# Optimization experiments

Hardware: AMD Instinct MI355X
Metric: run time of the kernel (lower is better)

Reference implementation:

```python
import jax, jax.numpy as jnp
import numpy as np

H = 8          # attention heads
EPS = 1e-5     # LayerNorm eps (torch default)
B, T, E = 8, 1024, 128
D, DI, N, DC, R = 512, 1024, 16, 4, 32   # d_model, d_inner, d_state, d_conv, dt_rank
NT, NM = 6, 8                            # transformer layers, mamba layers
FF = 2048                                # transformer dim_feedforward (torch default)


def setup_inputs():
    key = jax.random.key(0)
    ks = iter(jax.random.split(key, 48))
    def rn(shape, scale=0.05):
        return jax.random.normal(next(ks), shape, jnp.float32) * scale
    return {
        "emb":      jax.random.normal(next(ks), (B, T, E), jnp.float32),
        # TransformerEncoder (6 post-norm layers), params stacked on leading layer dim
        "t_wqkv":   rn((NT, 3 * E, E)), "t_bqkv": jnp.zeros((NT, 3 * E), jnp.float32),
        "t_wo":     rn((NT, E, E)),     "t_bo":   jnp.zeros((NT, E), jnp.float32),
        "t_ln1w":   jnp.ones((NT, E), jnp.float32),  "t_ln1b": jnp.zeros((NT, E), jnp.float32),
        "t_w1":     rn((NT, FF, E)),    "t_b1":   jnp.zeros((NT, FF), jnp.float32),
        "t_w2":     rn((NT, E, FF)),    "t_b2":   jnp.zeros((NT, E), jnp.float32),
        "t_ln2w":   jnp.ones((NT, E), jnp.float32),  "t_ln2b": jnp.zeros((NT, E), jnp.float32),
        # Linear(emb_dim -> d_model)
        "w_in":     rn((D, E)), "b_in": jnp.zeros((D,), jnp.float32),
        # MambaBlocks (8 raw Mamba layers, no residual/norm), stacked
        "m_inproj": rn((NM, 2 * DI, D)),
        "m_convw":  rn((NM, DI, DC), 0.2), "m_convb": jnp.zeros((NM, DI), jnp.float32),
        "m_xproj":  rn((NM, R + 2 * N, DI)),
        "m_dtw":    rn((NM, DI, R), 0.1),
        "m_dtb":    jax.random.uniform(next(ks), (NM, DI), jnp.float32, -6.0, -3.0),
        "m_Alog":   jnp.log(jnp.tile(jnp.arange(1, N + 1, dtype=jnp.float32), (NM, DI, 1))),
        "m_D":      jnp.ones((NM, DI), jnp.float32),
        "m_outproj": rn((NM, D, DI)),
        # Linear(d_model -> emb_dim)
        "w_out":    rn((E, D)), "b_out": jnp.zeros((E,), jnp.float32),
    }


def _ln(x, w, b):
    mu = jnp.mean(x, -1, keepdims=True)
    var = jnp.var(x, -1, keepdims=True)
    return (x - mu) * jax.lax.rsqrt(var + EPS) * w + b


def _tlayer(x, p):
    wqkv, bqkv, wo, bo, ln1w, ln1b, w1, b1, w2, b2, ln2w, ln2b = p
    qkv = x @ wqkv.T + bqkv                        # (B,T,3E)
    q, k, v = jnp.split(qkv, 3, axis=-1)
    def heads(t):                                  # (B,T,E) -> (B,H,T,E//H)
        return t.reshape(B, T, H, E // H).transpose(0, 2, 1, 3)
    q, k, v = heads(q), heads(k), heads(v)
    scores = jnp.einsum("bhqd,bhkd->bhqk", q, k) / jnp.sqrt(jnp.float32(E // H))
    attn = jax.nn.softmax(scores, axis=-1)
    o = jnp.einsum("bhqk,bhkd->bhqd", attn, v).transpose(0, 2, 1, 3).reshape(B, T, E)
    x = _ln(x + o @ wo.T + bo, ln1w, ln1b)         # post-norm (torch default)
    ff = jax.nn.relu(x @ w1.T + b1) @ w2.T + b2
    return _ln(x + ff, ln2w, ln2b)


def _mamba_layer(x, p):
    inproj, convw, convb, xproj, dtw, dtb, Alog, Dp, outproj = p
    xz = x @ inproj.T                              # (B,T,2*DI)
    xi, z = jnp.split(xz, 2, axis=-1)
    # causal depthwise conv1d, kernel DC, left-padded
    xp = jnp.pad(xi, ((0, 0), (DC - 1, 0), (0, 0)))
    conv = sum(xp[:, k:k + T, :] * convw[:, k] for k in range(DC)) + convb
    xi = jax.nn.silu(conv)
    dbc = xi @ xproj.T                             # (B,T,R+2N)
    dt_r, Bt, Ct = dbc[..., :R], dbc[..., R:R + N], dbc[..., R + N:]
    dt = jax.nn.softplus(dt_r @ dtw.T + dtb)       # (B,T,DI)
    A = -jnp.exp(Alog)                             # (DI,N)
    def step(h, inputs):
        dt_t, B_t, C_t, x_t = inputs               # (B,DI),(B,N),(B,N),(B,DI)
        dA = jnp.exp(dt_t[:, :, None] * A)         # (B,DI,N)
        h = h * dA + (dt_t * x_t)[:, :, None] * B_t[:, None, :]
        y = jnp.einsum("bdn,bn->bd", h, C_t)
        return h, y
    h0 = jnp.zeros((B, DI, N), x.dtype)
    seq = (dt.transpose(1, 0, 2), Bt.transpose(1, 0, 2),
           Ct.transpose(1, 0, 2), xi.transpose(1, 0, 2))
    _, ys = jax.lax.scan(step, h0, seq)            # ys: (T,B,DI)
    y = ys.transpose(1, 0, 2) + Dp * xi
    y = y * jax.nn.silu(z)
    return y @ outproj.T                           # (B,T,D)


def reference(emb, t_wqkv, t_bqkv, t_wo, t_bo, t_ln1w, t_ln1b, t_w1, t_b1, t_w2, t_b2,
              t_ln2w, t_ln2b, w_in, b_in, m_inproj, m_convw, m_convb, m_xproj, m_dtw,
              m_dtb, m_Alog, m_D, m_outproj, w_out, b_out):
    x = emb
    tparams = (t_wqkv, t_bqkv, t_wo, t_bo, t_ln1w, t_ln1b, t_w1, t_b1, t_w2, t_b2, t_ln2w, t_ln2b)
    for i in range(NT):
        x = _tlayer(x, tuple(p[i] for p in tparams))
    x = x @ w_in.T + b_in                          # (B,T,D)
    mparams = (m_inproj, m_convw, m_convb, m_xproj, m_dtw, m_dtb, m_Alog, m_D, m_outproj)
    for i in range(NM):
        x = _mamba_layer(x, tuple(p[i] for p in mparams))
    return x @ w_out.T + b_out                     # (B,T,E)
```

## Files before the change

### kernel.cpp

```cpp
#include <hip/hip_runtime.h>
#include <math.h>

#define HB 8
#define TT 1024
#define NSTATE 16
#define NTT 6
#define NMM 8
#define MM (HB*TT)
#define EPSV 1e-5f
#define CHUNK 64
#define NCH (TT/CHUNK)
#define LSTR 72
#define AKS 128
#define VSTR 132

typedef _Float16 f16x8 __attribute__((ext_vector_type(8)));
typedef _Float16 f16x4 __attribute__((ext_vector_type(4)));
typedef float f32x4_t __attribute__((ext_vector_type(4)));

static __device__ inline void split8(const float4 a, const float4 b,
                                     f16x8& h, f16x8& l)
{
  float x[8] = {a.x, a.y, a.z, a.w, b.x, b.y, b.z, b.w};
#pragma unroll
  for (int i = 0; i < 8; i++) {
    _Float16 hi = (_Float16)x[i];
    h[i] = hi;
    l[i] = (_Float16)(x[i] - (float)hi);
  }
}

template<int TN>
__global__ __launch_bounds__(256) void gemm_mfma_t(
    const float* __restrict__ A, int lda,
    const float* __restrict__ W,
    const float* __restrict__ bias,
    float* __restrict__ C,
    float* __restrict__ P,
    int N, int K, int S, int act)
{
  __shared__ _Float16 As[128 * LSTR];
  __shared__ _Float16 Bs[TN * LSTR];
  const int tid = threadIdx.x;
  const int m0 = blockIdx.y * 128;
  const int n0 = blockIdx.x * TN;
  const int z = blockIdx.z;
  const int kchunk = K / S;
  const int kb = z * kchunk;
  const int ke = kb + kchunk;

  const int lr = tid >> 1;
  const int lh = tid & 1;
  const int lane = tid & 63;
  const int w = tid >> 6;
  const int quad = lane >> 4;
  const int l16 = lane & 15;

  const float* Arow = A + (size_t)(m0 + lr) * lda + lh * 16;
  _Float16* Adst = &As[lr * LSTR + lh * 16];

  constexpr int MI = (TN == 128) ? 4 : 2;
  const int w0 = (TN == 128) ? (w & 1) : w;
  const int w1 = (TN == 128) ? (w >> 1) : 0;
  const int rowbase = (TN == 128) ? w0 * 64 : w0 * 32;

  f32x4_t acc[MI][4];
#pragma unroll
  for (int i = 0; i < MI; i++)
#pragma unroll
    for (int j = 0; j < 4; j++)
#pragma unroll
      for (int r = 0; r < 4; r++) acc[i][j][r] = 0.f;

  const _Float16* ab = &As[(rowbase + l16) * LSTR + quad * 8];
  const _Float16* bb = &Bs[(w1 * 64 + l16) * LSTR + quad * 8];

  const float* Wrow;
  _Float16* Bdst;
  if (TN == 128) {
    Wrow = W + (size_t)(n0 + lr) * K + lh * 16;
    Bdst = &Bs[lr * LSTR + lh * 16];
  } else {
    const int br = tid >> 2;
    const int bo = (tid & 3) * 8;
    Wrow = W + (size_t)(n0 + br) * K + bo;
    Bdst = &Bs[br * LSTR + bo];
  }

  for (int k0 = kb; k0 < ke; k0 += 32) {
    float4 a0 = *(const float4*)&Arow[k0];
    float4 a1 = *(const float4*)&Arow[k0 + 4];
    float4 a2 = *(const float4*)&Arow[k0 + 8];
    float4 a3 = *(const float4*)&Arow[k0 + 12];
    float4 b0 = *(const float4*)&Wrow[k0];
    float4 b1 = *(const float4*)&Wrow[k0 + 4];
    float4 b2, b3;
    if (TN == 128) {
      b2 = *(const float4*)&Wrow[k0 + 8];
      b3 = *(const float4*)&Wrow[k0 + 12];
    }
    __syncthreads();
    {
      f16x8 h, l;
      split8(a0, a1, h, l);
      *(f16x8*)&Adst[0] = h; *(f16x8*)&Adst[32] = l;
      split8(a2, a3, h, l);
      *(f16x8*)&Adst[8] = h; *(f16x8*)&Adst[40] = l;
      split8(b0, b1, h, l);
      *(f16x8*)&Bdst[0] = h; *(f16x8*)&Bdst[32] = l;
      if (TN == 128) {
        split8(b2, b3, h, l);
        *(f16x8*)&Bdst[8] = h; *(f16x8*)&Bdst[40] = l;
      }
    }
    __syncthreads();

    f16x8 bh[4], bl[4];
#pragma unroll
    for (int ni = 0; ni < 4; ni++) {
      bh[ni] = *(const f16x8*)&bb[ni * 16 * LSTR];
      bl[ni] = *(const f16x8*)&bb[ni * 16 * LSTR + 32];
    }
#pragma unroll
    for (int mi = 0; mi < MI; mi++) {
      f16x8 ah = *(const f16x8*)&ab[mi * 16 * LSTR];
      f16x8 al = *(const f16x8*)&ab[mi * 16 * LSTR + 32];
#pragma unroll
      for (int ni = 0; ni < 4; ni++) {
        acc[mi][ni] = __builtin_amdgcn_mfma_f32_16x16x32_f16(ah, bh[ni], acc[mi][ni], 0, 0, 0);
        acc[mi][ni] = __builtin_amdgcn_mfma_f32_16x16x32_f16(ah, bl[ni], acc[mi][ni], 0, 0, 0);
        acc[mi][ni] = __builtin_amdgcn_mfma_f32_16x16x32_f16(al, bh[ni], acc[mi][ni], 0, 0, 0);
      }
    }
  }

  float* dst = (S == 1) ? C : (P + (size_t)z * MM * N);
#pragma unroll
  for (int ni = 0; ni < 4; ni++) {
    const int n = n0 + w1 * 64 + ni * 16 + l16;
    const float bv = (S == 1 && bias) ? bias[n] : 0.f;
#pragma unroll
    for (int mi = 0; mi < MI; mi++) {
      const int mbase = m0 + rowbase + mi * 16 + quad * 4;
#pragma unroll
      for (int r = 0; r < 4; r++) {
        float v = acc[mi][ni][r] + bv;
        if (S == 1) {
          if (act == 1) v = fmaxf(v, 0.f);
          else if (act == 2) v = fmaxf(v, 0.f) + log1pf(__expf(-fabsf(v)));
        }
        dst[(size_t)(mbase + r) * N + n] = v;
      }
    }
  }
}

__global__ __launch_bounds__(256) void reduce_k(
    const float* __restrict__ P, const float* __restrict__ bias,
    float* __restrict__ C, int nmask, int S, int act, int stride4)
{
  const int idx = blockIdx.x * 256 + threadIdx.x;
  float4 a = *(const float4*)&P[(size_t)idx * 4];
  for (int z = 1; z < S; z++) {
    float4 p = *(const float4*)&P[(size_t)(idx + z * (size_t)stride4) * 4];
    a.x += p.x; a.y += p.y; a.z += p.z; a.w += p.w;
  }
  if (bias) {
    float4 bv = *(const float4*)&bias[(idx * 4) & nmask];
    a.x += bv.x; a.y += bv.y; a.z += bv.z; a.w += bv.w;
  }
  if (act == 1) {
    a.x = fmaxf(a.x, 0.f); a.y = fmaxf(a.y, 0.f);
    a.z = fmaxf(a.z, 0.f); a.w = fmaxf(a.w, 0.f);
  } else if (act == 2) {
    a.x = fmaxf(a.x, 0.f) + log1pf(__expf(-fabsf(a.x)));
    a.y = fmaxf(a.y, 0.f) + log1pf(__expf(-fabsf(a.y)));
    a.z = fmaxf(a.z, 0.f) + log1pf(__expf(-fabsf(a.z)));
    a.w = fmaxf(a.w, 0.f) + log1pf(__expf(-fabsf(a.w)));
  }
  *(float4*)&C[(size_t)idx * 4] = a;
}

__global__ __launch_bounds__(256) void attn_mfma_k(
    const float* __restrict__ qkv, float* __restrict__ o)
{
  __shared__ _Float16 Khi[AKS * 16], Klo[AKS * 16];
  __shared__ _Float16 Vthi[16 * VSTR], Vtlo[16 * VSTR];
  __shared__ float Pscr[4][16 * 18];

  const int tid = threadIdx.x;
  const int lane = tid & 63;
  const int wv = tid >> 6;
  const int quad = lane >> 4;
  const int l16 = lane & 15;
  const int qh = quad & 1;
  const int bh = blockIdx.y;
  const int b = bh >> 3;
  const int h = bh & 7;
  const int qb0 = blockIdx.x * 128;

  f16x8 qa[2];
#pragma unroll
  for (int u = 0; u < 2; u++) {
    const int qrow = qb0 + wv * 32 + u * 16 + l16;
    const float* qp = qkv + (size_t)(b * TT + qrow) * 384 + h * 16 + qh * 8;
    float4 x0 = *(const float4*)&qp[0];
    float4 x1 = *(const float4*)&qp[4];
    float xv[8] = {x0.x, x0.y, x0.z, x0.w, x1.x, x1.y, x1.z, x1.w};
#pragma unroll
    for (int j = 0; j < 8; j++) {
      float q = xv[j] * 0.25f;
      _Float16 hi = (_Float16)q;
      _Float16 lo = (_Float16)(q - (float)hi);
      qa[u][j] = (quad < 2) ? hi : lo;
    }
  }

  f32x4_t oacc[2];
  float lacc[2][4];
#pragma unroll
  for (int u = 0; u < 2; u++)
#pragma unroll
    for (int r = 0; r < 4; r++) { oacc[u][r] = 0.f; lacc[u][r] = 0.f; }

  float* Pw = &Pscr[wv][0];

  for (int ks = 0; ks < TT; ks += AKS) {
    __syncthreads();
    {
      const int key = tid >> 1, hf = tid & 1;
      const float* kp = qkv + (size_t)(b * TT + ks + key) * 384 + 128 + h * 16 + hf * 8;
      float4 k0 = *(const float4*)&kp[0];
      float4 k1 = *(const float4*)&kp[4];
      f16x8 vh, vl;
      split8(k0, k1, vh, vl);
      *(f16x8*)&Khi[key * 16 + hf * 8] = vh;
      *(f16x8*)&Klo[key * 16 + hf * 8] = vl;
      const float* vp = kp + 128;
      float4 v0 = *(const float4*)&vp[0];
      float4 v1 = *(const float4*)&vp[4];
      float vvv[8] = {v0.x, v0.y, v0.z, v0.w, v1.x, v1.y, v1.z, v1.w};
#pragma unroll
      for (int j = 0; j < 8; j++) {
        const int d = hf * 8 + j;
        _Float16 hi = (_Float16)vvv[j];
        Vthi[d * VSTR + key] = hi;
        Vtlo[d * VSTR + key] = (_Float16)(vvv[j] - (float)hi);
      }
    }
    __syncthreads();

    for (int kt = 0; kt < AKS; kt += 16) {
      f16x8 kfh = *(const f16x8*)&Khi[(kt + l16) * 16 + qh * 8];
      f16x8 kfl = *(const f16x8*)&Klo[(kt + l16) * 16 + qh * 8];
      const int vo = l16 * VSTR + kt + qh * 8;
      f16x4 va0 = *(const f16x4*)&Vthi[vo];
      f16x4 va1 = *(const f16x4*)&Vthi[vo + 4];
      f16x4 vb0 = *(const f16x4*)&Vtlo[vo];
      f16x4 vb1 = *(const f16x4*)&Vtlo[vo + 4];
      f16x8 vfh, vfl;
#pragma unroll
      for (int i = 0; i < 4; i++) {
        vfh[i] = va0[i]; vfh[4 + i] = va1[i];
        vfl[i] = vb0[i]; vfl[4 + i] = vb1[i];
      }

#pragma unroll
      for (int u = 0; u < 2; u++) {
        f32x4_t s;
#pragma unroll
        for (int r = 0; r < 4; r++) s[r] = 0.f;
        s = __builtin_amdgcn_mfma_f32_16x16x32_f16(qa[u], kfh, s, 0, 0, 0);
        s = __builtin_amdgcn_mfma_f32_16x16x32_f16(qa[u], kfl, s, 0, 0, 0);
        float p[4];
#pragma unroll
        for (int r = 0; r < 4; r++) {
          p[r] = __expf(s[r]);
          lacc[u][r] += p[r];
        }
        float* ps = Pw + (quad * 4) * 18 + l16;
        ps[0] = p[0]; ps[18] = p[1]; ps[36] = p[2]; ps[54] = p[3];
        __asm__ volatile("s_waitcnt lgkmcnt(0)" ::: "memory");
        const float* pr = Pw + l16 * 18 + qh * 8;
        f16x8 pa;
#pragma unroll
        for (int j = 0; j < 8; j++) {
          float pv = pr[j];
          _Float16 hi = (_Float16)pv;
          _Float16 lo = (_Float16)(pv - (float)hi);
          pa[j] = (quad < 2) ? hi : lo;
        }
        oacc[u] = __builtin_amdgcn_mfma_f32_16x16x32_f16(pa, vfh, oacc[u], 0, 0, 0);
        oacc[u] = __builtin_amdgcn_mfma_f32_16x16x32_f16(pa, vfl, oacc[u], 0, 0, 0);
        __asm__ volatile("s_waitcnt lgkmcnt(0)" ::: "memory");
      }
    }
  }

#pragma unroll
  for (int u = 0; u < 2; u++) {
#pragma unroll
    for (int r = 0; r < 4; r++) {
      float lv = lacc[u][r];
      lv += __shfl_xor(lv, 1);
      lv += __shfl_xor(lv, 2);
      lv += __shfl_xor(lv, 4);
      lv += __shfl_xor(lv, 8);
      const float inv = 1.f / lv;
      const int qrow = qb0 + wv * 32 + u * 16 + quad * 4 + r;
      o[(size_t)(b * TT + qrow) * 128 + h * 16 + l16] = oacc[u][r] * inv;
    }
  }
}

__global__ __launch_bounds__(256) void add_ln_k(
    const float* __restrict__ a, const float* __restrict__ bvec,
    const float* __restrict__ w, const float* __restrict__ bb,
    float* __restrict__ out)
{
  const int tid = threadIdx.x;
  const int wave = tid >> 6, lane = tid & 63;
  const size_t row = (size_t)blockIdx.x * 4 + wave;
  const float* pa = a + row * 128;
  const float* pb = bvec + row * 128;
  float v0 = pa[lane] + pb[lane];
  float v1 = pa[lane + 64] + pb[lane + 64];
  float s1 = v0 + v1, s2 = v0 * v0 + v1 * v1;
#pragma unroll
  for (int off = 32; off; off >>= 1) {
    s1 += __shfl_down(s1, off);
    s2 += __shfl_down(s2, off);
  }
  s1 = __shfl(s1, 0); s2 = __shfl(s2, 0);
  const float mean = s1 * (1.f / 128.f);
  const float var = s2 * (1.f / 128.f) - mean * mean;
  const float rs = rsqrtf(var + EPSV);
  out[row * 128 + lane]      = (v0 - mean) * rs * w[lane] + bb[lane];
  out[row * 128 + lane + 64] = (v1 - mean) * rs * w[lane + 64] + bb[lane + 64];
}

__global__ __launch_bounds__(256) void conv_silu_k(
    const float* __restrict__ xz, const float* __restrict__ cw,
    const float* __restrict__ cb, float* __restrict__ out)
{
  const int idx = blockIdx.x * 256 + threadIdx.x;
  const int di = idx & 1023;
  const int m = idx >> 10;
  const int t = m & (TT - 1);
  float acc = cb[di];
#pragma unroll
  for (int k = 0; k < 4; k++) {
    int tt = t + k - 3;
    if (tt >= 0) acc += xz[(size_t)(m + k - 3) * 2048 + di] * cw[di * 4 + k];
  }
  out[(size_t)m * 1024 + di] = acc / (1.f + __expf(-acc));
}

__global__ __launch_bounds__(64) void scan_partial_k(
    const float* __restrict__ dt,
    const float* __restrict__ dbc,
    const float* __restrict__ xi,
    const float* __restrict__ Alog,
    float* __restrict__ Pb, float* __restrict__ Sb)
{
  const int slice = blockIdx.x & 15;
  const int c = blockIdx.x >> 4;
  const int b = blockIdx.y;
  const int di = slice * 64 + threadIdx.x;

  float A[NSTATE];
#pragma unroll
  for (int n = 0; n < NSTATE; n++) A[n] = -__expf(Alog[di * NSTATE + n]);
  float h[NSTATE], P[NSTATE];
#pragma unroll
  for (int n = 0; n < NSTATE; n++) { h[n] = 0.f; P[n] = 1.f; }

  const size_t m0 = (size_t)b * TT + (size_t)c * CHUNK;
  for (int t = 0; t < CHUNK; t++) {
    const size_t m = m0 + t;
    const float dtv = dt[m * 1024 + di];
    const float xv  = xi[m * 1024 + di];
    const float dtx = dtv * xv;
#pragma unroll
    for (int n = 0; n < NSTATE; n++) {
      const float Bv = dbc[m * 64 + 32 + n];
      const float dA = __expf(dtv * A[n]);
      h[n] = h[n] * dA + dtx * Bv;
      P[n] *= dA;
    }
  }
  const size_t base = (((size_t)b * NCH + c) * NSTATE) * 1024 + di;
#pragma unroll
  for (int n = 0; n < NSTATE; n++) {
    Pb[base + (size_t)n * 1024] = P[n];
    Sb[base + (size_t)n * 1024] = h[n];
  }
}

__global__ __launch_bounds__(256) void scan_fix_k(
    float* __restrict__ Pb, const float* __restrict__ Sb)
{
  const int idx = blockIdx.x * 256 + threadIdx.x;
  const int b = idx >> 10;
  const int di = idx & 1023;
  float h[NSTATE];
#pragma unroll
  for (int n = 0; n < NSTATE; n++) h[n] = 0.f;
  for (int c = 0; c < NCH; c++) {
    const size_t base = (((size_t)b * NCH + c) * NSTATE) * 1024 + di;
    float P[NSTATE], S[NSTATE];
#pragma unroll
    for (int n = 0; n < NSTATE; n++) {
      P[n] = Pb[base + (size_t)n * 1024];
      S[n] = Sb[base + (size_t)n * 1024];
    }
#pragma unroll
    for (int n = 0; n < NSTATE; n++) {
      Pb[base + (size_t)n * 1024] = h[n];
      h[n] = P[n] * h[n] + S[n];
    }
  }
}

__global__ __launch_bounds__(64) void scan_final_k(
    const float* __restrict__ dt,
    const float* __restrict__ dbc,
    const float* __restrict__ xi,
    const float* __restrict__ xz,
    const float* __restrict__ Alog,
    const float* __restrict__ Dp,
    const float* __restrict__ Hin,
    float* __restrict__ Y)
{
  const int slice = blockIdx.x & 15;
  const int c = blockIdx.x >> 4;
  const int b = blockIdx.y;
  const int di = slice * 64 + threadIdx.x;

  float A[NSTATE];
#pragma unroll
  for (int n = 0; n < NSTATE; n++) A[n] = -__expf(Alog[di * NSTATE + n]);
  const float Dv = Dp[di];
  float h[NSTATE];
  const size_t hbase = (((size_t)b * NCH + c) * NSTATE) * 1024 + di;
#pragma unroll
  for (int n = 0; n < NSTATE; n++) h[n] = Hin[hbase + (size_t)n * 1024];

  const size_t m0 = (size_t)b * TT + (size_t)c * CHUNK;
  for (int t = 0; t < CHUNK; t++) {
    const size_t m = m0 + t;
    const float dtv = dt[m * 1024 + di];
    const float xv  = xi[m * 1024 + di];
    const float zv  = xz[m * 2048 + 1024 + di];
    const float dtx = dtv * xv;
    float y = 0.f;
#pragma unroll
    for (int n = 0; n < NSTATE; n++) {
      const float Bv = dbc[m * 64 + 32 + n];
      const float Cv = dbc[m * 64 + 48 + n];
      const float dA = __expf(dtv * A[n]);
      h[n] = h[n] * dA + dtx * Bv;
      y += h[n] * Cv;
    }
    y += Dv * xv;
    y *= zv / (1.f + __expf(-zv));
    Y[m * 1024 + di] = y;
  }
}

extern "C" void kernel_launch(void* const* d_in, const int* in_sizes, int n_in,
                              void* d_out, int out_size, void* d_ws, size_t ws_size,
                              hipStream_t stream)
{
  const float* emb      = (const float*)d_in[0];
  const float* t_wqkv   = (const float*)d_in[1];
  const float* t_bqkv   = (const float*)d_in[2];
  const float* t_wo     = (const float*)d_in[3];
  const float* t_bo     = (const float*)d_in[4];
  const float* t_ln1w   = (const float*)d_in[5];
  const float* t_ln1b   = (const float*)d_in[6];
  const float* t_w1     = (const float*)d_in[7];
  const float* t_b1     = (const float*)d_in[8];
  const float* t_w2     = (const float*)d_in[9];
  const float* t_b2     = (const float*)d_in[10];
  const float* t_ln2w   = (const float*)d_in[11];
  const float* t_ln2b   = (const float*)d_in[12];
  const float* w_in     = (const float*)d_in[13];
  const float* b_in     = (const float*)d_in[14];
  const float* m_inproj = (const float*)d_in[15];
  const float* m_convw  = (const float*)d_in[16];
  const float* m_convb  = (const float*)d_in[17];
  const float* m_xproj  = (const float*)d_in[18];
  const float* m_dtw    = (const float*)d_in[19];
  const float* m_dtb    = (const float*)d_in[20];
  const float* m_Alog   = (const float*)d_in[21];
  const float* m_D      = (const float*)d_in[22];
  const float* m_outproj= (const float*)d_in[23];
  const float* w_out    = (const float*)d_in[24];
  const float* b_out    = (const float*)d_in[25];

  float* ws = (float*)d_ws;
  float* X0   = ws;
  float* X1   = X0 + (size_t)MM * 512;
  float* Abuf = X1 + (size_t)MM * 512;
  float* Bf   = Abuf + (size_t)MM * 2048;
  float* Cf   = Bf + (size_t)MM * 1024;
  float* Yb   = Cf + (size_t)MM * 1024;
  float* Db   = Yb + (size_t)MM * 1024;

  dim3 blk(256);
  auto gemm = [&](const float* A, int lda, const float* W, const float* bias,
                  float* C, int N, int K, int act, int S, float* P, bool tn64) {
    dim3 g(N / (tn64 ? 64 : 128), MM / 128, S);
    if (tn64)
      hipLaunchKernelGGL(gemm_mfma_t<64>, g, blk, 0, stream,
                         A, lda, W, S == 1 ? bias : nullptr, C, P, N, K, S, act);
    else
      hipLaunchKernelGGL(gemm_mfma_t<128>, g, blk, 0, stream,
                         A, lda, W, S == 1 ? bias : nullptr, C, P, N, K, S, act);
    if (S > 1) {
      int stride4 = (MM * N) / 4;
      hipLaunchKernelGGL(reduce_k, dim3(stride4 / 256), blk, 0, stream,
                         P, bias, C, N - 1, S, act, stride4);
    }
  };

  const float* x = emb;
  for (int l = 0; l < NTT; l++) {
    gemm(x, 128, t_wqkv + (size_t)l * 384 * 128, t_bqkv + l * 384,
         Abuf, 384, 128, 0, 1, nullptr, false);
    hipLaunchKernelGGL(attn_mfma_k, dim3(TT / 128, HB * 8), blk, 0, stream,
                       Abuf, Yb);
    gemm(Yb, 128, t_wo + (size_t)l * 128 * 128, t_bo + l * 128,
         Cf, 128, 128, 0, 2, X1, true);
    hipLaunchKernelGGL(add_ln_k, dim3(MM / 4), blk, 0, stream,
                       x, Cf, t_ln1w + l * 128, t_ln1b + l * 128, X0);
    gemm(X0, 128, t_w1 + (size_t)l * 2048 * 128, t_b1 + l * 2048,
         Abuf, 2048, 128, 1, 1, nullptr, false);
    gemm(Abuf, 2048, t_w2 + (size_t)l * 128 * 2048, t_b2 + l * 128,
         Cf, 128, 2048, 0, 8, Yb, false);
    hipLaunchKernelGGL(add_ln_k, dim3(MM / 4), blk, 0, stream,
                       X0, Cf, t_ln2w + l * 128, t_ln2b + l * 128, X0);
    x = X0;
  }

  gemm(X0, 128, w_in, b_in, X1, 512, 128, 0, 1, nullptr, false);

  float* xc = X1;
  float* xo = X0;
  for (int l = 0; l < NMM; l++) {
    gemm(xc, 512, m_inproj + (size_t)l * 2048 * 512, nullptr,
         Abuf, 2048, 512, 0, 1, nullptr, false);
    hipLaunchKernelGGL(conv_silu_k, dim3(MM * 1024 / 256), blk, 0, stream,
                       Abuf, m_convw + (size_t)l * 1024 * 4, m_convb + l * 1024, Bf);
    gemm(Bf, 1024, m_xproj + (size_t)l * 64 * 1024, nullptr,
         Db, 64, 1024, 0, 4, xo, true);
    gemm(Db, 64, m_dtw + (size_t)l * 1024 * 32, m_dtb + l * 1024,
         Cf, 1024, 32, 2, 1, nullptr, false);

    float* Pb = xo;
    float* Sb = xo + (size_t)HB * NCH * NSTATE * 1024;
    hipLaunchKernelGGL(scan_partial_k, dim3(16 * NCH, HB), dim3(64), 0, stream,
                       Cf, Db, Bf, m_Alog + (size_t)l * 1024 * 16, Pb, Sb);
    hipLaunchKernelGGL(scan_fix_k, dim3(MM / 1024 * 4), blk, 0, stream, Pb, Sb);
    hipLaunchKernelGGL(scan_final_k, dim3(16 * NCH, HB), dim3(64), 0, stream,
                       Cf, Db, Bf, Abuf,
                       m_Alog + (size_t)l * 1024 * 16, m_D + l * 1024, Pb, Yb);

    gemm(Yb, 1024, m_outproj + (size_t)l * 512 * 1024, nullptr,
         xo, 512, 1024, 0, 2, Abuf, false);
    float* tmp = xc; xc = xo; xo = tmp;
  }

  gemm(xc, 512, w_out, b_out, (float*)d_out, 128, 512, 0, 4, Yb, false);
}
```

Baseline: 3.623 ms.

## Pre-split GEMM operands into swizzled fp16 hi/lo tiles loaded via global_load_lds

Instead of each GEMM converting fp32 A and W tiles into fp16 hi/lo pairs inside the main loop, producers (attention, layernorm, conv, scan, reduce, GEMM epilogue) now write their outputs directly in a pre-split, XOR-swizzled fp16 tile layout, and weights are split by separate split kernels. The GEMM then streams tiles straight into LDS with global_load_lds and does no conversion in its inner loop. The workspace is reorganized into aliased regions. This removes per-tile conversion ALU work and register staging, at the cost of extra split-kernel launches, double-written outputs, and delicate buffer aliasing.

```diff
diff --git a/kernel.cpp b/kernel.cpp
--- a/kernel.cpp
+++ b/kernel.cpp
@@ -10,7 +10,6 @@
 #define EPSV 1e-5f
 #define CHUNK 64
 #define NCH (TT/CHUNK)
-#define LSTR 72
 #define AKS 128
 #define VSTR 132
 
@@ -18,8 +17,8 @@
 typedef _Float16 f16x4 __attribute__((ext_vector_type(4)));
 typedef float f32x4_t __attribute__((ext_vector_type(4)));
 
-static __device__ inline void split8(const float4 a, const float4 b,
-                                     f16x8& h, f16x8& l)
+static __device__ __forceinline__ void split8(const float4 a, const float4 b,
+                                              f16x8& h, f16x8& l)
 {
   float x[8] = {a.x, a.y, a.z, a.w, b.x, b.y, b.z, b.w};
 #pragma unroll
@@ -30,34 +29,90 @@
   }
 }
 
+static __device__ __forceinline__ void gload16(const _Float16* g, _Float16* l)
+{
+  __builtin_amdgcn_global_load_lds(
+      (const __attribute__((address_space(1))) unsigned int*)g,
+      (__attribute__((address_space(3))) unsigned int*)l, 16, 0, 0);
+}
+
+static __device__ __forceinline__ void store_split(_Float16* __restrict__ dst,
+                                                   size_t row, int col, float v)
+{
+  const int cc = col & 31;
+  const size_t o = ((size_t)(col >> 5) * MM + row) * 64
+                 + (size_t)(((((cc >> 3) ^ ((int)row & 7)) * 8)) + (cc & 7));
+  _Float16 hi = (_Float16)v;
+  dst[o] = hi;
+  dst[o ^ (size_t)32] = (_Float16)(v - (float)hi);
+}
+
+static __device__ __forceinline__ void split_item(
+    const float* __restrict__ src, int lda, int rows,
+    _Float16* __restrict__ dst, int item)
+{
+  const int m = item % rows;
+  const int seg = item / rows;
+  const float* s = src + (size_t)m * lda + seg * 32;
+  _Float16* d = dst + (size_t)item * 64;
+  const int swz = m & 7;
+#pragma unroll
+  for (int g = 0; g < 4; g++) {
+    float4 x0 = *(const float4*)&s[g * 8];
+    float4 x1 = *(const float4*)&s[g * 8 + 4];
+    f16x8 h, l;
+    split8(x0, x1, h, l);
+    const int u = (g ^ swz) * 8;
+    *(f16x8*)&d[u] = h;
+    *(f16x8*)&d[u ^ 32] = l;
+  }
+}
+
+__global__ __launch_bounds__(256) void split_k(
+    const float* __restrict__ src, int lda, int rows,
+    _Float16* __restrict__ dst)
+{
+  split_item(src, lda, rows, dst, blockIdx.x * 256 + threadIdx.x);
+}
+
+__global__ __launch_bounds__(256) void split3_k(
+    const float* __restrict__ s0, int lda0, int rows0, _Float16* __restrict__ d0, int nb0,
+    const float* __restrict__ s1, int lda1, int rows1, _Float16* __restrict__ d1, int nb1,
+    const float* __restrict__ s2, int lda2, int rows2, _Float16* __restrict__ d2)
+{
+  const int bid = blockIdx.x;
+  if (bid < nb0) {
+    split_item(s0, lda0, rows0, d0, bid * 256 + threadIdx.x);
+  } else if (bid < nb0 + nb1) {
+    split_item(s1, lda1, rows1, d1, (bid - nb0) * 256 + threadIdx.x);
+  } else {
+    split_item(s2, lda2, rows2, d2, (bid - nb0 - nb1) * 256 + threadIdx.x);
+  }
+}
+
 template<int TN>
-__global__ __launch_bounds__(256) void gemm_mfma_t(
-    const float* __restrict__ A, int lda,
-    const float* __restrict__ W,
+__global__ __launch_bounds__(256, 4) void gemm_ps_t(
+    const _Float16* __restrict__ Ap, int astr,
+    const _Float16* __restrict__ Wp, int wstr,
     const float* __restrict__ bias,
     float* __restrict__ C,
     float* __restrict__ P,
+    _Float16* __restrict__ Cs,
     int N, int K, int S, int act)
 {
-  __shared__ _Float16 As[128 * LSTR];
-  __shared__ _Float16 Bs[TN * LSTR];
+  __shared__ __align__(16) _Float16 As[128 * 64];
+  __shared__ __align__(16) _Float16 Bs[TN * 64];
   const int tid = threadIdx.x;
-  const int m0 = blockIdx.y * 128;
-  const int n0 = blockIdx.x * TN;
-  const int z = blockIdx.z;
-  const int kchunk = K / S;
-  const int kb = z * kchunk;
-  const int ke = kb + kchunk;
-
-  const int lr = tid >> 1;
-  const int lh = tid & 1;
   const int lane = tid & 63;
   const int w = tid >> 6;
   const int quad = lane >> 4;
   const int l16 = lane & 15;
-
-  const float* Arow = A + (size_t)(m0 + lr) * lda + lh * 16;
-  _Float16* Adst = &As[lr * LSTR + lh * 16];
+  const int m0 = blockIdx.y * 128;
+  const int n0 = blockIdx.x * TN;
+  const int z = blockIdx.z;
+  const int nseg = K / 32;
+  const int segb = z * (nseg / S);
+  const int sege = segb + nseg / S;
 
   constexpr int MI = (TN == 128) ? 4 : 2;
   const int w0 = (TN == 128) ? (w & 1) : w;
@@ -72,59 +127,33 @@
 #pragma unroll
       for (int r = 0; r < 4; r++) acc[i][j][r] = 0.f;
 
-  const _Float16* ab = &As[(rowbase + l16) * LSTR + quad * 8];
-  const _Float16* bb = &Bs[(w1 * 64 + l16) * LSTR + quad * 8];
-
-  const float* Wrow;
-  _Float16* Bdst;
-  if (TN == 128) {
-    Wrow = W + (size_t)(n0 + lr) * K + lh * 16;
-    Bdst = &Bs[lr * LSTR + lh * 16];
-  } else {
-    const int br = tid >> 2;
-    const int bo = (tid & 3) * 8;
-    Wrow = W + (size_t)(n0 + br) * K + bo;
-    Bdst = &Bs[br * LSTR + bo];
-  }
-
-  for (int k0 = kb; k0 < ke; k0 += 32) {
-    float4 a0 = *(const float4*)&Arow[k0];
-    float4 a1 = *(const float4*)&Arow[k0 + 4];
-    float4 a2 = *(const float4*)&Arow[k0 + 8];
-    float4 a3 = *(const float4*)&Arow[k0 + 12];
-    float4 b0 = *(const float4*)&Wrow[k0];
-    float4 b1 = *(const float4*)&Wrow[k0 + 4];
-    float4 b2, b3;
-    if (TN == 128) {
-      b2 = *(const float4*)&Wrow[k0 + 8];
-      b3 = *(const float4*)&Wrow[k0 + 12];
-    }
+  const int sw8 = (quad ^ (l16 & 7)) * 8;
+  const int abase = (rowbase + l16) * 64 + sw8;
+  const int bbase = (w1 * 64 + l16) * 64 + sw8;
+  const int wave64 = tid & 192;
+
+  for (int seg = segb; seg < sege; seg++) {
+    const _Float16* At = Ap + ((size_t)seg * astr + m0) * 64;
+    const _Float16* Bt = Wp + ((size_t)seg * wstr + n0) * 64;
     __syncthreads();
-    {
-      f16x8 h, l;
-      split8(a0, a1, h, l);
-      *(f16x8*)&Adst[0] = h; *(f16x8*)&Adst[32] = l;
-      split8(a2, a3, h, l);
-      *(f16x8*)&Adst[8] = h; *(f16x8*)&Adst[40] = l;
-      split8(b0, b1, h, l);
-      *(f16x8*)&Bdst[0] = h; *(f16x8*)&Bdst[32] = l;
-      if (TN == 128) {
-        split8(b2, b3, h, l);
-        *(f16x8*)&Bdst[8] = h; *(f16x8*)&Bdst[40] = l;
-      }
-    }
+#pragma unroll
+    for (int j = 0; j < 4; j++)
+      gload16(At + (size_t)(j * 256 + tid) * 8, &As[(j * 256 + wave64) * 8]);
+#pragma unroll
+    for (int j = 0; j < TN / 32; j++)
+      gload16(Bt + (size_t)(j * 256 + tid) * 8, &Bs[(j * 256 + wave64) * 8]);
     __syncthreads();
 
     f16x8 bh[4], bl[4];
 #pragma unroll
     for (int ni = 0; ni < 4; ni++) {
-      bh[ni] = *(const f16x8*)&bb[ni * 16 * LSTR];
-      bl[ni] = *(const f16x8*)&bb[ni * 16 * LSTR + 32];
+      bh[ni] = *(const f16x8*)&Bs[bbase + ni * 1024];
+      bl[ni] = *(const f16x8*)&Bs[(bbase ^ 32) + ni * 1024];
     }
 #pragma unroll
     for (int mi = 0; mi < MI; mi++) {
-      f16x8 ah = *(const f16x8*)&ab[mi * 16 * LSTR];
-      f16x8 al = *(const f16x8*)&ab[mi * 16 * LSTR + 32];
+      f16x8 ah = *(const f16x8*)&As[abase + mi * 1024];
+      f16x8 al = *(const f16x8*)&As[(abase ^ 32) + mi * 1024];
 #pragma unroll
       for (int ni = 0; ni < 4; ni++) {
         acc[mi][ni] = __builtin_amdgcn_mfma_f32_16x16x32_f16(ah, bh[ni], acc[mi][ni], 0, 0, 0);
@@ -149,7 +178,12 @@
           if (act == 1) v = fmaxf(v, 0.f);
           else if (act == 2) v = fmaxf(v, 0.f) + log1pf(__expf(-fabsf(v)));
         }
-        dst[(size_t)(mbase + r) * N + n] = v;
+        const int row = mbase + r;
+        if (S == 1 && Cs) {
+          store_split(Cs, (size_t)row, n, v);
+        } else {
+          dst[(size_t)row * N + n] = v;
+        }
       }
     }
   }
@@ -157,12 +191,14 @@
 
 __global__ __launch_bounds__(256) void reduce_k(
     const float* __restrict__ P, const float* __restrict__ bias,
-    float* __restrict__ C, int nmask, int S, int act, int stride4)
+    float* __restrict__ C, _Float16* __restrict__ Cs,
+    _Float16* __restrict__ dta,
+    int nmask, int nshift, int S, int act, int stride4)
 {
   const int idx = blockIdx.x * 256 + threadIdx.x;
   float4 a = *(const float4*)&P[(size_t)idx * 4];
   for (int z = 1; z < S; z++) {
-    float4 p = *(const float4*)&P[(size_t)(idx + z * (size_t)stride4) * 4];
+    float4 p = *(const float4*)&P[(size_t)(idx + (size_t)z * stride4) * 4];
     a.x += p.x; a.y += p.y; a.z += p.z; a.w += p.w;
   }
   if (bias) {
@@ -178,11 +214,26 @@
     a.z = fmaxf(a.z, 0.f) + log1pf(__expf(-fabsf(a.z)));
     a.w = fmaxf(a.w, 0.f) + log1pf(__expf(-fabsf(a.w)));
   }
-  *(float4*)&C[(size_t)idx * 4] = a;
+  const int c0 = (idx * 4) & nmask;
+  const size_t row = (size_t)(idx * 4) >> nshift;
+  if (Cs) {
+    store_split(Cs, row, c0,     a.x);
+    store_split(Cs, row, c0 + 1, a.y);
+    store_split(Cs, row, c0 + 2, a.z);
+    store_split(Cs, row, c0 + 3, a.w);
+  } else {
+    *(float4*)&C[(size_t)idx * 4] = a;
+  }
+  if (dta && c0 < 32) {
+    store_split(dta, row, c0,     a.x);
+    store_split(dta, row, c0 + 1, a.y);
+    store_split(dta, row, c0 + 2, a.z);
+    store_split(dta, row, c0 + 3, a.w);
+  }
 }
 
 __global__ __launch_bounds__(256) void attn_mfma_k(
-    const float* __restrict__ qkv, float* __restrict__ o)
+    const float* __restrict__ qkv, _Float16* __restrict__ os)
 {
   __shared__ _Float16 Khi[AKS * 16], Klo[AKS * 16];
   __shared__ _Float16 Vthi[16 * VSTR], Vtlo[16 * VSTR];
@@ -308,7 +359,8 @@
       lv += __shfl_xor(lv, 8);
       const float inv = 1.f / lv;
       const int qrow = qb0 + wv * 32 + u * 16 + quad * 4 + r;
-      o[(size_t)(b * TT + qrow) * 128 + h * 16 + l16] = oacc[u][r] * inv;
+      const size_t m = (size_t)(b * TT + qrow);
+      store_split(os, m, h * 16 + l16, oacc[u][r] * inv);
     }
   }
 }
@@ -316,7 +368,7 @@
 __global__ __launch_bounds__(256) void add_ln_k(
     const float* __restrict__ a, const float* __restrict__ bvec,
     const float* __restrict__ w, const float* __restrict__ bb,
-    float* __restrict__ out)
+    float* __restrict__ out, _Float16* __restrict__ outs)
 {
   const int tid = threadIdx.x;
   const int wave = tid >> 6, lane = tid & 63;
@@ -335,13 +387,18 @@
   const float mean = s1 * (1.f / 128.f);
   const float var = s2 * (1.f / 128.f) - mean * mean;
   const float rs = rsqrtf(var + EPSV);
-  out[row * 128 + lane]      = (v0 - mean) * rs * w[lane] + bb[lane];
-  out[row * 128 + lane + 64] = (v1 - mean) * rs * w[lane + 64] + bb[lane + 64];
+  const float o0 = (v0 - mean) * rs * w[lane] + bb[lane];
+  const float o1 = (v1 - mean) * rs * w[lane + 64] + bb[lane + 64];
+  out[row * 128 + lane] = o0;
+  out[row * 128 + lane + 64] = o1;
+  store_split(outs, row, lane, o0);
+  store_split(outs, row, lane + 64, o1);
 }
 
 __global__ __launch_bounds__(256) void conv_silu_k(
     const float* __restrict__ xz, const float* __restrict__ cw,
-    const float* __restrict__ cb, float* __restrict__ out)
+    const float* __restrict__ cb, float* __restrict__ out,
+    _Float16* __restrict__ outs)
 {
   const int idx = blockIdx.x * 256 + threadIdx.x;
   const int di = idx & 1023;
@@ -353,7 +410,9 @@
     int tt = t + k - 3;
     if (tt >= 0) acc += xz[(size_t)(m + k - 3) * 2048 + di] * cw[di * 4 + k];
   }
-  out[(size_t)m * 1024 + di] = acc / (1.f + __expf(-acc));
+  const float y = acc / (1.f + __expf(-acc));
+  out[(size_t)m * 1024 + di] = y;
+  store_split(outs, (size_t)m, di, y);
 }
 
 __global__ __launch_bounds__(64) void scan_partial_k(
@@ -430,7 +489,7 @@
     const float* __restrict__ Alog,
     const float* __restrict__ Dp,
     const float* __restrict__ Hin,
-    float* __restrict__ Y)
+    _Float16* __restrict__ Y)
 {
   const int slice = blockIdx.x & 15;
   const int c = blockIdx.x >> 4;
@@ -464,7 +523,7 @@
     }
     y += Dv * xv;
     y *= zv / (1.f + __expf(-zv));
-    Y[m * 1024 + di] = y;
+    store_split(Y, m, di, y);
   }
 }
 
@@ -472,6 +531,7 @@
                               void* d_out, int out_size, void* d_ws, size_t ws_size,
                               hipStream_t stream)
 {
+  (void)in_sizes; (void)n_in; (void)out_size; (void)ws_size;
   const float* emb      = (const float*)d_in[0];
   const float* t_wqkv   = (const float*)d_in[1];
   const float* t_bqkv   = (const float*)d_in[2];
@@ -500,77 +560,116 @@
   const float* b_out    = (const float*)d_in[25];
 
   float* ws = (float*)d_ws;
-  float* X0   = ws;
-  float* X1   = X0 + (size_t)MM * 512;
-  float* Abuf = X1 + (size_t)MM * 512;
-  float* Bf   = Abuf + (size_t)MM * 2048;
-  float* Cf   = Bf + (size_t)MM * 1024;
-  float* Yb   = Cf + (size_t)MM * 1024;
-  float* Db   = Yb + (size_t)MM * 1024;
+  float* R1 = ws;
+  float* R2 = ws + (size_t)MM * 512;
+  float* R3 = ws + (size_t)MM * 1024;
+  float* R4 = ws + (size_t)MM * 3072;
+  float* R5 = ws + (size_t)MM * 4096;
+  float* R6 = ws + (size_t)MM * 5120;
+  float* R7 = ws + (size_t)MM * 6144;
+
+  _Float16* TWQKV = (_Float16*)R4;
+  _Float16* TWO   = TWQKV + (size_t)294912 * 2;
+  _Float16* TW1   = TWO   + (size_t)98304 * 2;
+  _Float16* TW2   = TW1   + (size_t)1572864 * 2;
+  _Float16* TWIN  = TW2   + (size_t)1572864 * 2;
+
+  _Float16* ASP1 = (_Float16*)R6;
+  _Float16* XIS  = (_Float16*)R6;
+  _Float16* DTA  = (_Float16*)R6;
+  _Float16* YSP  = (_Float16*)R6;
 
   dim3 blk(256);
-  auto gemm = [&](const float* A, int lda, const float* W, const float* bias,
-                  float* C, int N, int K, int act, int S, float* P, bool tn64) {
+  auto split = [&](const float* src, int lda, int rows, int K, _Float16* dst) {
+    hipLaunchKernelGGL(split_k, dim3(rows * (K / 32) / 256), blk, 0, stream,
+                       src, lda, rows, dst);
+  };
+  auto gemm = [&](const _Float16* Ap, const _Float16* Wp, int wstr,
+                  const float* bias, float* C, int N, int K, int act,
+                  int S, float* P, _Float16* Cs, _Float16* dta, bool tn64) {
     dim3 g(N / (tn64 ? 64 : 128), MM / 128, S);
     if (tn64)
-      hipLaunchKernelGGL(gemm_mfma_t<64>, g, blk, 0, stream,
-                         A, lda, W, S == 1 ? bias : nullptr, C, P, N, K, S, act);
+      hipLaunchKernelGGL(gemm_ps_t<64>, g, blk, 0, stream,
+                         Ap, MM, Wp, wstr, bias, C, P, Cs, N, K, S, act);
     else
-      hipLaunchKernelGGL(gemm_mfma_t<128>, g, blk, 0, stream,
-                         A, lda, W, S == 1 ? bias : nullptr, C, P, N, K, S, act);
+      hipLaunchKernelGGL(gemm_ps_t<128>, g, blk, 0, stream,
+                         Ap, MM, Wp, wstr, bias, C, P, Cs, N, K, S, act);
     if (S > 1) {
-      int stride4 = (MM * N) / 4;
+      int stride4 = (int)((size_t)MM * N / 4);
       hipLaunchKernelGGL(reduce_k, dim3(stride4 / 256), blk, 0, stream,
-                         P, bias, C, N - 1, S, act, stride4);
+                         P, bias, C, Cs, dta, N - 1, __builtin_ctz(N), S, act,
+                         stride4);
     }
   };
+
+  split(t_wqkv, 128,  2304,  128, TWQKV);
+  split(t_wo,   128,   768,  128, TWO);
+  split(t_w1,   128, 12288,  128, TW1);
+  split(t_w2,  2048,   768, 2048, TW2);
+  split(w_in,   128,   512,  128, TWIN);
+  split(emb,    128,    MM,  128, ASP1);
 
   const float* x = emb;
   for (int l = 0; l < NTT; l++) {
-    gemm(x, 128, t_wqkv + (size_t)l * 384 * 128, t_bqkv + l * 384,
-         Abuf, 384, 128, 0, 1, nullptr, false);
+    gemm(ASP1, TWQKV + (size_t)l * 384 * 64, 2304, t_bqkv + l * 384,
+         R3, 384, 128, 0, 1, nullptr, nullptr, nullptr, false);
     hipLaunchKernelGGL(attn_mfma_k, dim3(TT / 128, HB * 8), blk, 0, stream,
-                       Abuf, Yb);
-    gemm(Yb, 128, t_wo + (size_t)l * 128 * 128, t_bo + l * 128,
-         Cf, 128, 128, 0, 2, X1, true);
+                       R3, ASP1);
+    gemm(ASP1, TWO + (size_t)l * 128 * 64, 768, t_bo + l * 128,
+         R5, 128, 128, 0, 2, R2, nullptr, nullptr, true);
     hipLaunchKernelGGL(add_ln_k, dim3(MM / 4), blk, 0, stream,
-                       x, Cf, t_ln1w + l * 128, t_ln1b + l * 128, X0);
-    gemm(X0, 128, t_w1 + (size_t)l * 2048 * 128, t_b1 + l * 2048,
-         Abuf, 2048, 128, 1, 1, nullptr, false);
-    gemm(Abuf, 2048, t_w2 + (size_t)l * 128 * 2048, t_b2 + l * 128,
-         Cf, 128, 2048, 0, 8, Yb, false);
+                       x, R5, t_ln1w + l * 128, t_ln1b + l * 128, R1, ASP1);
+    gemm(ASP1, TW1 + (size_t)l * 2048 * 64, 12288, t_b1 + l * 2048,
+         R3, 2048, 128, 1, 1, nullptr, (_Float16*)R3, nullptr, false);
+    gemm((_Float16*)R3, TW2 + (size_t)l * 128 * 64, 768, t_b2 + l * 128,
+         R5, 128, 2048, 0, 8, R6, nullptr, nullptr, false);
     hipLaunchKernelGGL(add_ln_k, dim3(MM / 4), blk, 0, stream,
-                       X0, Cf, t_ln2w + l * 128, t_ln2b + l * 128, X0);
-    x = X0;
-  }
-
-  gemm(X0, 128, w_in, b_in, X1, 512, 128, 0, 1, nullptr, false);
-
-  float* xc = X1;
-  float* xo = X0;
+                       R1, R5, t_ln2w + l * 128, t_ln2b + l * 128, R1, ASP1);
+    x = R1;
+  }
+
+  gemm(ASP1, TWIN, 512, b_in, R2, 512, 128, 0, 1, nullptr, (_Float16*)R2,
+       nullptr, false);
+
+  float* xcs = R2;
+  float* xos = R1;
   for (int l = 0; l < NMM; l++) {
-    gemm(xc, 512, m_inproj + (size_t)l * 2048 * 512, nullptr,
-         Abuf, 2048, 512, 0, 1, nullptr, false);
+    _Float16* WIs = (_Float16*)(xos + (size_t)MM * 256);
+    _Float16* WXs = (_Float16*)(xos + (size_t)MM * 384);
+    _Float16* WDs = (_Float16*)(xos + (size_t)MM * 392);
+    _Float16* WOs = (_Float16*)(xos + (size_t)MM * 256);
+    hipLaunchKernelGGL(split3_k, dim3(140), blk, 0, stream,
+        m_inproj + (size_t)l * 2048 * 512, 512, 2048, WIs, 128,
+        m_xproj  + (size_t)l * 64 * 1024, 1024,   64, WXs,   8,
+        m_dtw    + (size_t)l * 1024 * 32,   32, 1024, WDs);
+
+    gemm((_Float16*)xcs, WIs, 2048, nullptr,
+         R3, 2048, 512, 0, 1, nullptr, nullptr, nullptr, false);
     hipLaunchKernelGGL(conv_silu_k, dim3(MM * 1024 / 256), blk, 0, stream,
-                       Abuf, m_convw + (size_t)l * 1024 * 4, m_convb + l * 1024, Bf);
-    gemm(Bf, 1024, m_xproj + (size_t)l * 64 * 1024, nullptr,
-         Db, 64, 1024, 0, 4, xo, true);
-    gemm(Db, 64, m_dtw + (size_t)l * 1024 * 32, m_dtb + l * 1024,
-         Cf, 1024, 32, 2, 1, nullptr, false);
-
-    float* Pb = xo;
-    float* Sb = xo + (size_t)HB * NCH * NSTATE * 1024;
+                       R3, m_convw + (size_t)l * 1024 * 4, m_convb + l * 1024,
+                       R4, XIS);
+    gemm(XIS, WXs, 64, nullptr,
+         R7, 64, 1024, 0, 4, xos, nullptr, DTA, true);
+    gemm(DTA, WDs, 1024, m_dtb + l * 1024,
+         R5, 1024, 32, 2, 1, nullptr, nullptr, nullptr, false);
+
+    float* Pb = xos;
+    float* Sb = xos + (size_t)MM * 256;
     hipLaunchKernelGGL(scan_partial_k, dim3(16 * NCH, HB), dim3(64), 0, stream,
-                       Cf, Db, Bf, m_Alog + (size_t)l * 1024 * 16, Pb, Sb);
+                       R5, R7, R4, m_Alog + (size_t)l * 1024 * 16, Pb, Sb);
     hipLaunchKernelGGL(scan_fix_k, dim3(MM / 1024 * 4), blk, 0, stream, Pb, Sb);
+    split(m_outproj + (size_t)l * 512 * 1024, 1024, 512, 1024, WOs);
     hipLaunchKernelGGL(scan_final_k, dim3(16 * NCH, HB), dim3(64), 0, stream,
-                       Cf, Db, Bf, Abuf,
-                       m_Alog + (size_t)l * 1024 * 16, m_D + l * 1024, Pb, Yb);
-
-    gemm(Yb, 1024, m_outproj + (size_t)l * 512 * 1024, nullptr,
-         xo, 512, 1024, 0, 2, Abuf, false);
-    float* tmp = xc; xc = xo; xo = tmp;
-  }
-
-  gemm(xc, 512, w_out, b_out, (float*)d_out, 128, 512, 0, 4, Yb, false);
-}
+                       R5, R7, R4, R3,
+                       m_Alog + (size_t)l * 1024 * 16, m_D + l * 1024, Pb, YSP);
+
+    gemm(YSP, WOs, 512, nullptr,
+         R5, 512, 1024, 0, 2, R3, (_Float16*)xos, nullptr, false);
+    float* ts = xcs; xcs = xos; xos = ts;
+  }
+
+  _Float16* WOUTs = (_Float16*)xos;
+  split(w_out, 512, 128, 512, WOUTs);
+  gemm((_Float16*)xcs, WOUTs, 128, b_out,
+       (float*)d_out, 128, 512, 0, 4, R6, nullptr, nullptr, false);
+}
```

Result: slower. 3.779 ms (+4.3%).
